# Optimization experiments

Measured on AMD Instinct MI355X. Metric: run time of the kernel, lower is better.

## Reference

```python
import jax, jax.numpy as jnp
import numpy as np

DIM = 1024
NUM_EXPERTS = 64
TOP_K = 8


def setup_inputs() -> dict:
    key = jax.random.key(0)
    kx, kw, kb = jax.random.split(key, 3)
    x = jax.random.normal(kx, (8, 4096, DIM), dtype=jnp.float32)
    # nn.Linear(dim, num_experts): weight [E, D], bias [E]
    bound = 1.0 / np.sqrt(DIM)
    W = jax.random.uniform(kw, (NUM_EXPERTS, DIM), minval=-bound, maxval=bound, dtype=jnp.float32)
    b = jax.random.uniform(kb, (NUM_EXPERTS,), minval=-bound, maxval=bound, dtype=jnp.float32)
    return {"x": x, "W": W, "b": b}


def reference(x, W, b):
    B, S, D = x.shape
    E = W.shape[0]
    # router logits: [B, S, E]
    logits = jnp.einsum("bsd,ed->bse", x, W) + b
    # top-k per token
    top_vals, indices = jax.lax.top_k(logits, TOP_K)  # [B,S,K]
    # scatter top-k logits into -inf tensor, then softmax
    flat_logits = logits.reshape(-1, E)
    flat_idx = indices.reshape(-1, TOP_K)
    flat_vals = top_vals.reshape(-1, TOP_K)
    rows = jnp.arange(flat_logits.shape[0])[:, None]
    sparse = jnp.full_like(flat_logits, -jnp.inf).at[rows, flat_idx].set(flat_vals)
    probs = jax.nn.softmax(sparse, axis=-1).reshape(B, S, E)
    return probs, indices
```

## Files before the change

kernel.cpp:

```cpp
#include <hip/hip_runtime.h>
#include <math.h>

#define DIM 1024
#define NEXP 64
#define TOPK 8
#define BM 128
#define KSPLIT 2
#define KHALF (DIM / KSPLIT)
#define BK 32
#define NCHUNK (KHALF / BK)
#define THREADS 256
#define LPAD 65

__device__ __forceinline__ void gload16(const float* g, float* l) {
    __builtin_amdgcn_global_load_lds(
        (const __attribute__((address_space(1))) void*)g,
        (__attribute__((address_space(3))) void*)l, 16, 0, 0);
}

__global__ __launch_bounds__(THREADS, 2)
void router_gemm_partial(const float* __restrict__ x,
                         const float* __restrict__ W,
                         float* __restrict__ part)
{
    __shared__ float x_s[2][BM][BK];
    __shared__ float w_s[2][NEXP][BK];

    const int tid  = threadIdx.x;
    const int trow = tid >> 4;
    const int tcol = tid & 15;
    const int tile = blockIdx.x;
    const int half = blockIdx.y;
    const int tok0 = tile * BM;
    const int k0   = half * KHALF;

    float acc[8][4];
#pragma unroll
    for (int i = 0; i < 8; ++i)
#pragma unroll
        for (int j = 0; j < 4; ++j) acc[i][j] = 0.f;

    const int rr = tid >> 3;
    const int c  = tid & 7;
    auto stage = [&](int buf, int kc) {
#pragma unroll
        for (int m = 0; m < 4; ++m) {
            int r  = m * 32 + rr;
            int cs = c ^ (r & 7);
            gload16(x + (size_t)(tok0 + r) * DIM + k0 + kc * BK + cs * 4,
                    &x_s[buf][r][c * 4]);
        }
#pragma unroll
        for (int m = 0; m < 2; ++m) {
            int r  = m * 32 + rr;
            int cs = c ^ (r & 7);
            gload16(W + (size_t)r * DIM + k0 + kc * BK + cs * 4,
                    &w_s[buf][r][c * 4]);
        }
    };

    auto compute = [&](int buf) {
#pragma unroll
        for (int k4 = 0; k4 < 8; ++k4) {
            const int cx = (k4 ^ (trow & 7)) * 4;
            const int cw = (k4 ^ (tcol & 7)) * 4;
            float4 xa[8], wa[4];
#pragma unroll
            for (int i = 0; i < 8; ++i)
                xa[i] = *(const float4*)&x_s[buf][trow + 16 * i][cx];
#pragma unroll
            for (int j = 0; j < 4; ++j)
                wa[j] = *(const float4*)&w_s[buf][tcol + 16 * j][cw];
#pragma unroll
            for (int i = 0; i < 8; ++i)
#pragma unroll
                for (int j = 0; j < 4; ++j) {
                    acc[i][j] = fmaf(xa[i].x, wa[j].x, acc[i][j]);
                    acc[i][j] = fmaf(xa[i].y, wa[j].y, acc[i][j]);
                    acc[i][j] = fmaf(xa[i].z, wa[j].z, acc[i][j]);
                    acc[i][j] = fmaf(xa[i].w, wa[j].w, acc[i][j]);
                }
        }
    };

    stage(0, 0);
    __syncthreads();
    for (int kc = 0; kc < NCHUNK; ++kc) {
        const int cur = kc & 1;
        if (kc + 1 < NCHUNK) stage(cur ^ 1, kc + 1);
        compute(cur);
        __syncthreads();
    }

    float* sstage = &x_s[0][0][0];
#pragma unroll
    for (int i = 0; i < 8; ++i)
#pragma unroll
        for (int j = 0; j < 4; ++j)
            sstage[(trow + 16 * i) * NEXP + tcol + 16 * j] = acc[i][j];
    __syncthreads();

    float* dst = part + ((size_t)(tile * KSPLIT + half) * BM) * NEXP;
#pragma unroll
    for (int it = 0; it < 8; ++it) {
        int v = tid + it * THREADS;
        *(float4*)(dst + v * 4) = *(const float4*)(sstage + v * 4);
    }
}

__global__ __launch_bounds__(THREADS, 1)
void router_topk_finalize(const float* __restrict__ part,
                          const float* __restrict__ b,
                          float* __restrict__ out_probs,
                          float* __restrict__ out_idx)
{
    __shared__ float logits_s[BM][LPAD];
    __shared__ float topk_s[BM][TOPK];

    const int tid  = threadIdx.x;
    const int tile = blockIdx.x;
    const int tok0 = tile * BM;

    const float* p0 = part + ((size_t)(tile * KSPLIT + 0) * BM) * NEXP;
    const float* p1 = part + ((size_t)(tile * KSPLIT + 1) * BM) * NEXP;

#pragma unroll
    for (int it = 0; it < 8; ++it) {
        int v = tid + it * THREADS;
        int r = v >> 4, c4 = (v & 15) * 4;
        float4 a = *(const float4*)(p0 + (size_t)r * NEXP + c4);
        float4 d = *(const float4*)(p1 + (size_t)r * NEXP + c4);
        float4 bv = *(const float4*)(b + c4);
        logits_s[r][c4 + 0] = a.x + d.x + bv.x;
        logits_s[r][c4 + 1] = a.y + d.y + bv.y;
        logits_s[r][c4 + 2] = a.z + d.z + bv.z;
        logits_s[r][c4 + 3] = a.w + d.w + bv.w;
    }
    __syncthreads();

    if (tid < BM) {
        const int t = tid;
        float pv[TOPK]; int pi[TOPK];
#pragma unroll
        for (int k = 0; k < TOPK; ++k) {
            float vmax = -INFINITY; int imax = 0;
#pragma unroll
            for (int e = 0; e < NEXP; ++e) {
                float v = logits_s[t][e];
                if (v > vmax) { vmax = v; imax = e; }
            }
            pv[k] = vmax; pi[k] = imax;
            logits_s[t][imax] = -INFINITY;
        }
        float p[TOPK]; float s = 0.f;
#pragma unroll
        for (int k = 0; k < TOPK; ++k) { p[k] = __expf(pv[k] - pv[0]); s += p[k]; }
        float inv = 1.f / s;

#pragma unroll
        for (int e = 0; e < NEXP; ++e) logits_s[t][e] = 0.f;
#pragma unroll
        for (int k = 0; k < TOPK; ++k) {
            logits_s[t][pi[k]] = p[k] * inv;
            topk_s[t][k] = (float)pi[k];
        }
    }
    __syncthreads();

#pragma unroll
    for (int it = 0; it < 8; ++it) {
        int v = tid + it * THREADS;
        int r = v >> 4, c4 = (v & 15) * 4;
        float4 z = make_float4(logits_s[r][c4], logits_s[r][c4 + 1],
                               logits_s[r][c4 + 2], logits_s[r][c4 + 3]);
        *(float4*)(out_probs + (size_t)(tok0 + r) * NEXP + c4) = z;
    }
    {
        int r = tid >> 1, c4 = tid & 1;
        float4 z = *(const float4*)&topk_s[r][c4 * 4];
        *(float4*)(out_idx + (size_t)(tok0 + r) * TOPK + c4 * 4) = z;
    }
}

extern "C" void kernel_launch(void* const* d_in, const int* in_sizes, int n_in,
                              void* d_out, int out_size, void* d_ws, size_t ws_size,
                              hipStream_t stream) {
    const float* x = (const float*)d_in[0];
    const float* W = (const float*)d_in[1];
    const float* b = (const float*)d_in[2];
    float* out = (float*)d_out;

    const int ntok = in_sizes[0] / DIM;
    float* out_probs = out;
    float* out_idx   = out + (size_t)ntok * NEXP;
    float* part      = (float*)d_ws;

    const int tiles = ntok / BM;
    router_gemm_partial<<<dim3(tiles, KSPLIT), THREADS, 0, stream>>>(x, W, part);
    router_topk_finalize<<<tiles, THREADS, 0, stream>>>(part, b, out_probs, out_idx);
}
```

Measured before the change: 235.2 us.

## Rework router GEMM tiling with 8x8 per-thread tiles and dynamic K-split

The GEMM kernel now runs 128 threads that each compute an 8x8 accumulator tile, using a 16-wide K chunk and a padded shared staging buffer for the output. The K dimension is split four ways when the workspace is large enough, otherwise two, which gives more blocks in flight. The finalize kernel handles 64 tokens per block and sums a variable number of partials. The aim is more arithmetic per shared-memory load and better occupancy. The cost is more partial-sum traffic and smaller K chunks, which means more barriers per block.

Result: slower. 253.2 us (+7.7%).

```diff
diff --git a/kernel.cpp b/kernel.cpp
--- a/kernel.cpp
+++ b/kernel.cpp
@@ -5,11 +5,10 @@
 #define NEXP 64
 #define TOPK 8
 #define BM 128
-#define KSPLIT 2
-#define KHALF (DIM / KSPLIT)
-#define BK 32
-#define NCHUNK (KHALF / BK)
-#define THREADS 256
+#define BK 16
+#define THREADS_G 128
+#define THREADS_F 256
+#define SPAD 68
 #define LPAD 65
 
 __device__ __forceinline__ void gload16(const float* g, float* l) {
@@ -18,127 +17,137 @@
         (__attribute__((address_space(3))) void*)l, 16, 0, 0);
 }
 
-__global__ __launch_bounds__(THREADS, 2)
+__global__ __launch_bounds__(THREADS_G, 2)
 void router_gemm_partial(const float* __restrict__ x,
                          const float* __restrict__ W,
-                         float* __restrict__ part)
+                         float* __restrict__ part,
+                         int ntok, int kq)
 {
-    __shared__ float x_s[2][BM][BK];
-    __shared__ float w_s[2][NEXP][BK];
+    __shared__ float smem[BM * SPAD];
+    float (*x_s)[BM][BK]   = (float (*)[BM][BK])smem;
+    float (*w_s)[NEXP][BK] = (float (*)[NEXP][BK])(smem + 4096);
 
     const int tid  = threadIdx.x;
-    const int trow = tid >> 4;
-    const int tcol = tid & 15;
-    const int tile = blockIdx.x;
+    const int trow = tid >> 3;
+    const int tcol = tid & 7;
+    const int lane = tid & 63;
+    const int wv   = tid >> 6;
+    const int tok0 = blockIdx.x * BM;
     const int half = blockIdx.y;
-    const int tok0 = tile * BM;
-    const int k0   = half * KHALF;
-
-    float acc[8][4];
+    const int k0   = half * kq;
+    const int nchunk = kq >> 4;
+
+    float acc[8][8];
 #pragma unroll
     for (int i = 0; i < 8; ++i)
 #pragma unroll
-        for (int j = 0; j < 4; ++j) acc[i][j] = 0.f;
-
-    const int rr = tid >> 3;
-    const int c  = tid & 7;
+        for (int j = 0; j < 8; ++j) acc[i][j] = 0.f;
+
+    const int rl = lane >> 2;
+    const int c  = lane & 3;
     auto stage = [&](int buf, int kc) {
+        const int kbase = k0 + kc * BK;
 #pragma unroll
         for (int m = 0; m < 4; ++m) {
-            int r  = m * 32 + rr;
-            int cs = c ^ (r & 7);
-            gload16(x + (size_t)(tok0 + r) * DIM + k0 + kc * BK + cs * 4,
+            int r  = wv * 64 + m * 16 + rl;
+            int cs = c ^ (r & 3);
+            gload16(x + (size_t)(tok0 + r) * DIM + kbase + cs * 4,
                     &x_s[buf][r][c * 4]);
         }
 #pragma unroll
         for (int m = 0; m < 2; ++m) {
-            int r  = m * 32 + rr;
-            int cs = c ^ (r & 7);
-            gload16(W + (size_t)r * DIM + k0 + kc * BK + cs * 4,
+            int r  = wv * 32 + m * 16 + rl;
+            int cs = c ^ (r & 3);
+            gload16(W + (size_t)r * DIM + kbase + cs * 4,
                     &w_s[buf][r][c * 4]);
         }
     };
 
     auto compute = [&](int buf) {
 #pragma unroll
-        for (int k4 = 0; k4 < 8; ++k4) {
-            const int cx = (k4 ^ (trow & 7)) * 4;
-            const int cw = (k4 ^ (tcol & 7)) * 4;
-            float4 xa[8], wa[4];
+        for (int k4 = 0; k4 < 4; ++k4) {
+            const int cx = (k4 ^ (trow & 3)) * 4;
+            const int cw = (k4 ^ (tcol & 3)) * 4;
+            float4 xa[8];
 #pragma unroll
             for (int i = 0; i < 8; ++i)
                 xa[i] = *(const float4*)&x_s[buf][trow + 16 * i][cx];
 #pragma unroll
-            for (int j = 0; j < 4; ++j)
-                wa[j] = *(const float4*)&w_s[buf][tcol + 16 * j][cw];
-#pragma unroll
-            for (int i = 0; i < 8; ++i)
-#pragma unroll
-                for (int j = 0; j < 4; ++j) {
-                    acc[i][j] = fmaf(xa[i].x, wa[j].x, acc[i][j]);
-                    acc[i][j] = fmaf(xa[i].y, wa[j].y, acc[i][j]);
-                    acc[i][j] = fmaf(xa[i].z, wa[j].z, acc[i][j]);
-                    acc[i][j] = fmaf(xa[i].w, wa[j].w, acc[i][j]);
-                }
+            for (int jh = 0; jh < 2; ++jh) {
+                float4 wa[4];
+#pragma unroll
+                for (int j = 0; j < 4; ++j)
+                    wa[j] = *(const float4*)&w_s[buf][tcol + 8 * (jh * 4 + j)][cw];
+#pragma unroll
+                for (int i = 0; i < 8; ++i)
+#pragma unroll
+                    for (int j = 0; j < 4; ++j) {
+                        float* a = &acc[i][jh * 4 + j];
+                        *a = fmaf(xa[i].x, wa[j].x, *a);
+                        *a = fmaf(xa[i].y, wa[j].y, *a);
+                        *a = fmaf(xa[i].z, wa[j].z, *a);
+                        *a = fmaf(xa[i].w, wa[j].w, *a);
+                    }
+            }
         }
     };
 
     stage(0, 0);
     __syncthreads();
-    for (int kc = 0; kc < NCHUNK; ++kc) {
+    for (int kc = 0; kc < nchunk; ++kc) {
         const int cur = kc & 1;
-        if (kc + 1 < NCHUNK) stage(cur ^ 1, kc + 1);
+        if (kc + 1 < nchunk) stage(cur ^ 1, kc + 1);
         compute(cur);
         __syncthreads();
     }
 
-    float* sstage = &x_s[0][0][0];
 #pragma unroll
     for (int i = 0; i < 8; ++i)
 #pragma unroll
-        for (int j = 0; j < 4; ++j)
-            sstage[(trow + 16 * i) * NEXP + tcol + 16 * j] = acc[i][j];
-    __syncthreads();
-
-    float* dst = part + ((size_t)(tile * KSPLIT + half) * BM) * NEXP;
-#pragma unroll
-    for (int it = 0; it < 8; ++it) {
-        int v = tid + it * THREADS;
-        *(float4*)(dst + v * 4) = *(const float4*)(sstage + v * 4);
-    }
-}
-
-__global__ __launch_bounds__(THREADS, 1)
+        for (int j = 0; j < 8; ++j)
+            smem[(trow + 16 * i) * SPAD + tcol + 8 * j] = acc[i][j];
+    __syncthreads();
+
+    float* dst = part + ((size_t)half * ntok + tok0) * NEXP;
+#pragma unroll
+    for (int it = 0; it < 16; ++it) {
+        int v = tid + it * THREADS_G;
+        int r = v >> 4, c4 = (v & 15) * 4;
+        *(float4*)(dst + (size_t)r * NEXP + c4) = *(const float4*)&smem[r * SPAD + c4];
+    }
+}
+
+__global__ __launch_bounds__(THREADS_F, 2)
 void router_topk_finalize(const float* __restrict__ part,
                           const float* __restrict__ b,
                           float* __restrict__ out_probs,
-                          float* __restrict__ out_idx)
+                          float* __restrict__ out_idx,
+                          int ntok, int ksplit)
 {
-    __shared__ float logits_s[BM][LPAD];
-    __shared__ float topk_s[BM][TOPK];
+    __shared__ float logits_s[64][LPAD];
+    __shared__ float topk_s[64][TOPK];
 
     const int tid  = threadIdx.x;
-    const int tile = blockIdx.x;
-    const int tok0 = tile * BM;
-
-    const float* p0 = part + ((size_t)(tile * KSPLIT + 0) * BM) * NEXP;
-    const float* p1 = part + ((size_t)(tile * KSPLIT + 1) * BM) * NEXP;
-
-#pragma unroll
-    for (int it = 0; it < 8; ++it) {
-        int v = tid + it * THREADS;
+    const int tok0 = blockIdx.x * 64;
+
+#pragma unroll
+    for (int it = 0; it < 4; ++it) {
+        int v = tid + it * THREADS_F;
         int r = v >> 4, c4 = (v & 15) * 4;
-        float4 a = *(const float4*)(p0 + (size_t)r * NEXP + c4);
-        float4 d = *(const float4*)(p1 + (size_t)r * NEXP + c4);
+        float4 s = make_float4(0.f, 0.f, 0.f, 0.f);
+        for (int h = 0; h < ksplit; ++h) {
+            float4 a = *(const float4*)(part + ((size_t)h * ntok + tok0 + r) * NEXP + c4);
+            s.x += a.x; s.y += a.y; s.z += a.z; s.w += a.w;
+        }
         float4 bv = *(const float4*)(b + c4);
-        logits_s[r][c4 + 0] = a.x + d.x + bv.x;
-        logits_s[r][c4 + 1] = a.y + d.y + bv.y;
-        logits_s[r][c4 + 2] = a.z + d.z + bv.z;
-        logits_s[r][c4 + 3] = a.w + d.w + bv.w;
-    }
-    __syncthreads();
-
-    if (tid < BM) {
+        logits_s[r][c4 + 0] = s.x + bv.x;
+        logits_s[r][c4 + 1] = s.y + bv.y;
+        logits_s[r][c4 + 2] = s.z + bv.z;
+        logits_s[r][c4 + 3] = s.w + bv.w;
+    }
+    __syncthreads();
+
+    if (tid < 64) {
         const int t = tid;
         float pv[TOPK]; int pi[TOPK];
 #pragma unroll
@@ -168,14 +177,14 @@
     __syncthreads();
 
 #pragma unroll
-    for (int it = 0; it < 8; ++it) {
-        int v = tid + it * THREADS;
+    for (int it = 0; it < 4; ++it) {
+        int v = tid + it * THREADS_F;
         int r = v >> 4, c4 = (v & 15) * 4;
         float4 z = make_float4(logits_s[r][c4], logits_s[r][c4 + 1],
                                logits_s[r][c4 + 2], logits_s[r][c4 + 3]);
         *(float4*)(out_probs + (size_t)(tok0 + r) * NEXP + c4) = z;
     }
-    {
+    if (tid < 128) {
         int r = tid >> 1, c4 = tid & 1;
         float4 z = *(const float4*)&topk_s[r][c4 * 4];
         *(float4*)(out_idx + (size_t)(tok0 + r) * TOPK + c4 * 4) = z;
@@ -195,7 +204,10 @@
     float* out_idx   = out + (size_t)ntok * NEXP;
     float* part      = (float*)d_ws;
 
-    const int tiles = ntok / BM;
-    router_gemm_partial<<<dim3(tiles, KSPLIT), THREADS, 0, stream>>>(x, W, part);
-    router_topk_finalize<<<tiles, THREADS, 0, stream>>>(part, b, out_probs, out_idx);
-}
+    const size_t need4 = (size_t)4 * ntok * NEXP * sizeof(float);
+    const int ksplit = (ws_size >= need4) ? 4 : 2;
+    const int kq = DIM / ksplit;
+
+    router_gemm_partial<<<dim3(ntok / BM, ksplit), THREADS_G, 0, stream>>>(x, W, part, ntok, kq);
+    router_topk_finalize<<<ntok / 64, THREADS_F, 0, stream>>>(part, b, out_probs, out_idx, ntok, ksplit);
+}
```
